# Performance work log

Hardware: AMD Instinct MI355X
Metric: run time of the kernel (lower is better)

Reference implementation:

```python
import jax, jax.numpy as jnp
import numpy as np

N_NODES = 100000
N_EDGES = 3200000
N_FEAT = 512
HIDDEN = 16
OUT_DIM = 1


def setup_inputs() -> dict:
    key = jax.random.key(0)
    ks = jax.random.split(key, 6)
    x = jax.random.normal(ks[0], (N_NODES, N_FEAT), dtype=jnp.float32)
    lap_vals = jax.random.uniform(ks[1], (N_EDGES,), dtype=jnp.float32)
    W1 = jax.random.normal(ks[2], (N_FEAT, HIDDEN), dtype=jnp.float32) * 0.05
    b1 = jnp.zeros((HIDDEN,), dtype=jnp.float32)
    W2 = jax.random.normal(ks[3], (HIDDEN, OUT_DIM), dtype=jnp.float32) * 0.05
    b2 = jnp.zeros((OUT_DIM,), dtype=jnp.float32)
    lap_rows = jax.random.randint(ks[4], (N_EDGES,), 0, N_NODES, dtype=jnp.int32)
    lap_cols = jax.random.randint(ks[5], (N_EDGES,), 0, N_NODES, dtype=jnp.int32)
    return {"x": x, "lap_vals": lap_vals, "W1": W1, "b1": b1,
            "W2": W2, "b2": b2, "lap_rows": lap_rows, "lap_cols": lap_cols}


def _spmm(vals, rows, cols, dense):
    # COO sparse [N,N] @ dense [N,D]: gather source rows, scale, scatter-add.
    return jax.ops.segment_sum(vals[:, None] * dense[cols], rows,
                               num_segments=N_NODES)


def reference(x, lap_vals, W1, b1, W2, b2, lap_rows, lap_cols):
    # Layer 1: dense GEMM -> sparse aggregation -> fused bias + relu
    h = jax.nn.relu(_spmm(lap_vals, lap_rows, lap_cols, x @ W1) + b1)
    # Layer 2: dense GEMM -> sparse aggregation -> fused bias + sigmoid
    out = jax.nn.sigmoid(_spmm(lap_vals, lap_rows, lap_cols, h @ W2) + b2)
    return out
```

## Files before the change

kernel.cpp:

```cpp
#include <hip/hip_runtime.h>
#include <cstdint>
#include <cstddef>

#define N_NODES 100000
#define N_EDGES 3200000
#define N_FEAT  512
#define HIDDEN  16
#define NBUCK   ((N_NODES + 127) / 128)
#define BCAP    5120
#define CHUNK   2048
#define NGB     ((N_NODES + 63) / 64)
#define NBS     ((N_EDGES + CHUNK - 1) / CHUNK)

static_assert(NGB == NBS, "parity interleave requires equal role counts");

__device__ __forceinline__ void gload_lds16(const float* g, void* lds) {
  __builtin_amdgcn_global_load_lds(
      (const __attribute__((address_space(1))) void*)g,
      (__attribute__((address_space(3))) void*)lds, 16, 0, 0);
}

__global__ __launch_bounds__(256)
void k_prep(int* __restrict__ cursor) {
  const int i = blockIdx.x * 256 + threadIdx.x;
  if (i < NBUCK) cursor[i] = 0;
}

__global__ __launch_bounds__(256)
void k_mega2(const float* __restrict__ x, const float* __restrict__ W1,
             float* __restrict__ xw, const int* __restrict__ rows,
             const int* __restrict__ cols, const float* __restrict__ vals,
             int* __restrict__ cursor, int2* __restrict__ binned) {
  __shared__ __align__(16) char smem[32768];
  const int t = threadIdx.x;

  if ((blockIdx.x & 1) == 0) {
    float4 (*xs)[2][256] = reinterpret_cast<float4 (*)[2][256]>(smem);
    const int l = t & 63;
    const int w = __builtin_amdgcn_readfirstlane(t >> 6);
    const int rbase = (blockIdx.x >> 1) * 64;
    const int kbase0 = w * 128;

    float acc[16];
#pragma unroll
    for (int c = 0; c < 16; ++c) acc[c] = 0.f;

    const int sq   = ((l & 3) ^ ((l >> 3) & 3)) * 4;
    const int srow = l >> 2;

    auto STAGE = [&](int b, int ck) {
      const int kb = kbase0 + ck * 16;
#pragma unroll
      for (int i = 0; i < 4; ++i) {
        int grow = rbase + i * 16 + srow;
        if (grow >= N_NODES) grow = N_NODES - 1;
        gload_lds16(x + (size_t)grow * N_FEAT + kb + sq, &xs[w][b][i * 64]);
      }
    };

    const int rsw = (l >> 1) & 3;
    auto COMPUTE = [&](int b, int ck) {
      const int kb = kbase0 + ck * 16;
#pragma unroll
      for (int q = 0; q < 4; ++q) {
        float4 xv = xs[w][b][l * 4 + (q ^ rsw)];
        float xe[4] = {xv.x, xv.y, xv.z, xv.w};
#pragma unroll
        for (int j = 0; j < 4; ++j) {
          const float* wrow = W1 + (size_t)(kb + q * 4 + j) * 16;
#pragma unroll
          for (int c = 0; c < 16; ++c)
            acc[c] = fmaf(xe[j], wrow[c], acc[c]);
        }
      }
    };

    STAGE(0, 0);
#pragma unroll 1
    for (int ck = 0; ck < 8; ++ck) {
      const int b = ck & 1;
      if (ck + 1 < 8) {
        STAGE(b ^ 1, ck + 1);
        asm volatile("s_waitcnt vmcnt(4)" ::: "memory");
      } else {
        asm volatile("s_waitcnt vmcnt(0)" ::: "memory");
      }
      COMPUTE(b, ck);
    }

    float4* red = &xs[w][0][0];
    red[l * 4 + 0] = make_float4(acc[0],  acc[1],  acc[2],  acc[3]);
    red[l * 4 + 1] = make_float4(acc[4],  acc[5],  acc[6],  acc[7]);
    red[l * 4 + 2] = make_float4(acc[8],  acc[9],  acc[10], acc[11]);
    red[l * 4 + 3] = make_float4(acc[12], acc[13], acc[14], acc[15]);
    __syncthreads();

    const int rr = t >> 2, qq = t & 3;
    const int grow = rbase + rr;
    if (grow < N_NODES) {
      const int s = rr * 4 + qq;
      float4 a = xs[0][0][s], b4 = xs[1][0][s], c4 = xs[2][0][s], d4 = xs[3][0][s];
      float4 o = make_float4(a.x + b4.x + c4.x + d4.x, a.y + b4.y + c4.y + d4.y,
                             a.z + b4.z + c4.z + d4.z, a.w + b4.w + c4.w + d4.w);
      ((float4*)xw)[(size_t)grow * 4 + qq] = o;
    }
  } else {
    int2*           stash = (int2*)smem;
    unsigned short* sbuck = (unsigned short*)(smem + 16384);
    int*            hist  = (int*)(smem + 16384 + 4096);
    int*            base  = (int*)(smem + 16384 + 4096 + 4 * NBUCK);
    const int e0 = (blockIdx.x >> 1) * CHUNK;
    const int nv = (N_EDGES - e0 < CHUNK) ? (N_EDGES - e0) : CHUNK;

    for (int b = t; b < NBUCK; b += 256) hist[b] = 0;
    __syncthreads();

#pragma unroll
    for (int i = 0; i < CHUNK / 256; ++i) {
      const int idx = i * 256 + t;
      if (idx < nv) {
        const int e = e0 + idx;
        const int r = rows[e], c = cols[e];
        const float v = vals[e];
        const int b = r >> 7;
        stash[idx] = make_int2(c | ((r & 127) << 20), __float_as_int(v));
        sbuck[idx] = (unsigned short)b;
        atomicAdd(&hist[b], 1);
      }
    }
    __syncthreads();

    for (int b = t; b < NBUCK; b += 256) {
      const int h = hist[b];
      base[b] = (h > 0) ? atomicAdd(&cursor[b], h) : 0;
      hist[b] = 0;
    }
    __syncthreads();

#pragma unroll
    for (int i = 0; i < CHUNK / 256; ++i) {
      const int idx = i * 256 + t;
      if (idx < nv) {
        const int b = sbuck[idx];
        const int off = base[b] + atomicAdd(&hist[b], 1);
        if (off < BCAP) binned[(size_t)b * BCAP + off] = stash[idx];
      }
    }
  }
}

__global__ __launch_bounds__(256)
void k_localcsr(const int2* __restrict__ binned, const int* __restrict__ cursor,
                int2* __restrict__ binned2, int* __restrict__ row_beg,
                int* __restrict__ row_end) {
  __shared__ unsigned short rk[BCAP];
  __shared__ int hist[128];
  __shared__ int pfx[128];
  const int t = threadIdx.x;
  const int b = blockIdx.x;
  const int raw = cursor[b];
  const int cnt = raw < BCAP ? raw : BCAP;
  const int2* ep = binned + (size_t)b * BCAP;
  int2* eq = binned2 + (size_t)b * BCAP;

  if (t < 128) hist[t] = 0;
  __syncthreads();

  for (int i = t; i < cnt; i += 256) {
    const int row = (ep[i].x >> 20) & 127;
    rk[i] = (unsigned short)atomicAdd(&hist[row], 1);
  }
  __syncthreads();

  if (t < 128) pfx[t] = hist[t];
  __syncthreads();
#pragma unroll
  for (int off = 1; off < 128; off <<= 1) {
    int add = (t >= off && t < 128) ? pfx[t - off] : 0;
    __syncthreads();
    if (t < 128) pfx[t] += add;
    __syncthreads();
  }

  if (t < 128) {
    const int r = b * 128 + t;
    if (r < N_NODES) {
      const int beg = b * BCAP + pfx[t] - hist[t];
      row_beg[r] = beg;
      row_end[r] = beg + hist[t];
    }
  }
  __syncthreads();

  for (int i = t; i < cnt; i += 256) {
    const int2 e = ep[i];
    const int row = (e.x >> 20) & 127;
    eq[pfx[row] - hist[row] + (int)rk[i]] = e;
  }
}

__global__ __launch_bounds__(256)
void k_fused1(const int2* __restrict__ binned2, const int* __restrict__ row_beg,
              const int* __restrict__ row_end, const float* __restrict__ xw,
              const float* __restrict__ b1, const float* __restrict__ W2,
              float* __restrict__ hw1) {
  const int t = threadIdx.x;
  const int lane16 = t & 15;
  const int r = blockIdx.x * 16 + (t >> 4);
  if (r >= N_NODES) return;
  const int s = row_beg[r], e = row_end[r];
  float a0 = 0.f, a1 = 0.f, a2 = 0.f, a3 = 0.f;
  int i = s;
  for (; i + 3 < e; i += 4) {
    int2 ea = binned2[i],     eb = binned2[i + 1];
    int2 ec = binned2[i + 2], ed = binned2[i + 3];
    a0 = fmaf(__int_as_float(ea.y), xw[(size_t)(ea.x & 0xFFFFF) * 16 + lane16], a0);
    a1 = fmaf(__int_as_float(eb.y), xw[(size_t)(eb.x & 0xFFFFF) * 16 + lane16], a1);
    a2 = fmaf(__int_as_float(ec.y), xw[(size_t)(ec.x & 0xFFFFF) * 16 + lane16], a2);
    a3 = fmaf(__int_as_float(ed.y), xw[(size_t)(ed.x & 0xFFFFF) * 16 + lane16], a3);
  }
  for (; i < e; ++i) {
    int2 ea = binned2[i];
    a0 = fmaf(__int_as_float(ea.y), xw[(size_t)(ea.x & 0xFFFFF) * 16 + lane16], a0);
  }
  float h = fmaxf((a0 + a1) + (a2 + a3) + b1[lane16], 0.f);
  float p = h * W2[lane16];
#pragma unroll
  for (int m = 8; m >= 1; m >>= 1) p += __shfl_xor(p, m, 16);
  if (lane16 == 0) hw1[r] = p;
}

__global__ __launch_bounds__(256)
void k_fused2(const int2* __restrict__ binned2, const int* __restrict__ row_beg,
              const int* __restrict__ row_end, const float* __restrict__ hw1,
              const float* __restrict__ b2, float* __restrict__ out) {
  const int t = threadIdx.x;
  const int lane16 = t & 15;
  const int r = blockIdx.x * 16 + (t >> 4);
  if (r >= N_NODES) return;
  const int s = row_beg[r], e = row_end[r];
  float acc = 0.f;
  for (int i = s + lane16; i < e; i += 16) {
    int2 ev = binned2[i];
    acc = fmaf(__int_as_float(ev.y), hw1[ev.x & 0xFFFFF], acc);
  }
#pragma unroll
  for (int m = 8; m >= 1; m >>= 1) acc += __shfl_xor(acc, m, 16);
  if (lane16 == 0) out[r] = 1.f / (1.f + expf(-(acc + b2[0])));
}

extern "C" void kernel_launch(void* const* d_in, const int* in_sizes, int n_in,
                              void* d_out, int out_size, void* d_ws, size_t ws_size,
                              hipStream_t stream) {
  const float* x    = (const float*)d_in[0];
  const float* vals = (const float*)d_in[1];
  const float* W1   = (const float*)d_in[2];
  const float* b1   = (const float*)d_in[3];
  const float* W2   = (const float*)d_in[4];
  const float* b2   = (const float*)d_in[5];
  const int*   rows = (const int*)d_in[6];
  const int*   cols = (const int*)d_in[7];
  float* out = (float*)d_out;

  char* w = (char*)d_ws;
  float* xw      = (float*)w;  w += (size_t)N_NODES * 16 * 4;
  int2*  binned  = (int2*)w;   w += (size_t)NBUCK * BCAP * 8;
  int2*  binned2 = (int2*)w;   w += (size_t)NBUCK * BCAP * 8;
  int*   cursor  = (int*)w;    w += (size_t)((NBUCK + 3) & ~3) * 4;
  int*   row_beg = (int*)w;    w += (size_t)N_NODES * 4;
  int*   row_end = (int*)w;    w += (size_t)N_NODES * 4;
  float* hw1     = (float*)w;

  k_prep    <<<(NBUCK + 255) / 256, 256, 0, stream>>>(cursor);
  k_mega2   <<<NGB + NBS,           256, 0, stream>>>(x, W1, xw, rows, cols, vals,
                                                      cursor, binned);
  k_localcsr<<<NBUCK,               256, 0, stream>>>(binned, cursor, binned2,
                                                      row_beg, row_end);
  k_fused1  <<<(N_NODES + 15) / 16, 256, 0, stream>>>(binned2, row_beg, row_end,
                                                      xw, b1, W2, hw1);
  k_fused2  <<<(N_NODES + 15) / 16, 256, 0, stream>>>(binned2, row_beg, row_end,
                                                      hw1, b2, out);
}
```

Measured before the change: 189.5 us.

## Fuse per-bucket CSR sort with layer-1 aggregation using LDS-staged edges

Merges the local CSR build and the first sparse aggregation into one kernel per 128-row bucket. Edges are sorted into an LDS stash and then aggregated straight from LDS, which removes one kernel launch and the global re-read of sorted edges. The sorted copy is still written to global memory for layer 2. It also shrinks the bucket capacity to 4608 so the int2 stash fits in LDS, which raises the risk of dropping edges in overfull buckets. The block grows to 512 threads, and only about 782 blocks now do the layer-1 gathers, so parallelism is lower.

```diff
diff --git a/kernel.cpp b/kernel.cpp
--- a/kernel.cpp
+++ b/kernel.cpp
@@ -7,10 +7,11 @@
 #define N_FEAT  512
 #define HIDDEN  16
 #define NBUCK   ((N_NODES + 127) / 128)
-#define BCAP    5120
+#define BCAP    4608
 #define CHUNK   2048
 #define NGB     ((N_NODES + 63) / 64)
 #define NBS     ((N_EDGES + CHUNK - 1) / CHUNK)
+#define AGG_T   512
 
 static_assert(NGB == NBS, "parity interleave requires equal role counts");
 
@@ -149,85 +150,87 @@
   }
 }
 
-__global__ __launch_bounds__(256)
-void k_localcsr(const int2* __restrict__ binned, const int* __restrict__ cursor,
-                int2* __restrict__ binned2, int* __restrict__ row_beg,
-                int* __restrict__ row_end) {
-  __shared__ unsigned short rk[BCAP];
+__global__ __launch_bounds__(AGG_T)
+void k_sortagg(const int2* __restrict__ binned, const int* __restrict__ cursor,
+               int2* __restrict__ binned2, int* __restrict__ row_beg,
+               int* __restrict__ row_end, const float* __restrict__ xw,
+               const float* __restrict__ b1, const float* __restrict__ W2,
+               float* __restrict__ hw1) {
+  __shared__ int2 stash[BCAP];
   __shared__ int hist[128];
-  __shared__ int pfx[128];
+  __shared__ int inc[128];
+  __shared__ int cnt2[128];
   const int t = threadIdx.x;
   const int b = blockIdx.x;
   const int raw = cursor[b];
   const int cnt = raw < BCAP ? raw : BCAP;
   const int2* ep = binned + (size_t)b * BCAP;
-  int2* eq = binned2 + (size_t)b * BCAP;
-
-  if (t < 128) hist[t] = 0;
-  __syncthreads();
-
-  for (int i = t; i < cnt; i += 256) {
-    const int row = (ep[i].x >> 20) & 127;
-    rk[i] = (unsigned short)atomicAdd(&hist[row], 1);
-  }
-  __syncthreads();
-
-  if (t < 128) pfx[t] = hist[t];
+
+  if (t < 128) { hist[t] = 0; cnt2[t] = 0; }
+  __syncthreads();
+
+  for (int i = t; i < cnt; i += AGG_T)
+    atomicAdd(&hist[(ep[i].x >> 20) & 127], 1);
+  __syncthreads();
+
+  if (t < 128) inc[t] = hist[t];
   __syncthreads();
 #pragma unroll
   for (int off = 1; off < 128; off <<= 1) {
-    int add = (t >= off && t < 128) ? pfx[t - off] : 0;
-    __syncthreads();
-    if (t < 128) pfx[t] += add;
+    int add = (t >= off && t < 128) ? inc[t - off] : 0;
+    __syncthreads();
+    if (t < 128) inc[t] += add;
     __syncthreads();
   }
 
   if (t < 128) {
     const int r = b * 128 + t;
     if (r < N_NODES) {
-      const int beg = b * BCAP + pfx[t] - hist[t];
-      row_beg[r] = beg;
-      row_end[r] = beg + hist[t];
-    }
-  }
-  __syncthreads();
-
-  for (int i = t; i < cnt; i += 256) {
+      row_beg[r] = b * BCAP + inc[t] - hist[t];
+      row_end[r] = b * BCAP + inc[t];
+    }
+  }
+
+  for (int i = t; i < cnt; i += AGG_T) {
     const int2 e = ep[i];
     const int row = (e.x >> 20) & 127;
-    eq[pfx[row] - hist[row] + (int)rk[i]] = e;
-  }
-}
-
-__global__ __launch_bounds__(256)
-void k_fused1(const int2* __restrict__ binned2, const int* __restrict__ row_beg,
-              const int* __restrict__ row_end, const float* __restrict__ xw,
-              const float* __restrict__ b1, const float* __restrict__ W2,
-              float* __restrict__ hw1) {
-  const int t = threadIdx.x;
+    const int off = inc[row] - hist[row] + atomicAdd(&cnt2[row], 1);
+    stash[off] = e;
+  }
+  __syncthreads();
+
+  int2* eq = binned2 + (size_t)b * BCAP;
+  for (int i = t; i < cnt; i += AGG_T) eq[i] = stash[i];
+
   const int lane16 = t & 15;
-  const int r = blockIdx.x * 16 + (t >> 4);
-  if (r >= N_NODES) return;
-  const int s = row_beg[r], e = row_end[r];
-  float a0 = 0.f, a1 = 0.f, a2 = 0.f, a3 = 0.f;
-  int i = s;
-  for (; i + 3 < e; i += 4) {
-    int2 ea = binned2[i],     eb = binned2[i + 1];
-    int2 ec = binned2[i + 2], ed = binned2[i + 3];
-    a0 = fmaf(__int_as_float(ea.y), xw[(size_t)(ea.x & 0xFFFFF) * 16 + lane16], a0);
-    a1 = fmaf(__int_as_float(eb.y), xw[(size_t)(eb.x & 0xFFFFF) * 16 + lane16], a1);
-    a2 = fmaf(__int_as_float(ec.y), xw[(size_t)(ec.x & 0xFFFFF) * 16 + lane16], a2);
-    a3 = fmaf(__int_as_float(ed.y), xw[(size_t)(ed.x & 0xFFFFF) * 16 + lane16], a3);
-  }
-  for (; i < e; ++i) {
-    int2 ea = binned2[i];
-    a0 = fmaf(__int_as_float(ea.y), xw[(size_t)(ea.x & 0xFFFFF) * 16 + lane16], a0);
-  }
-  float h = fmaxf((a0 + a1) + (a2 + a3) + b1[lane16], 0.f);
-  float p = h * W2[lane16];
-#pragma unroll
-  for (int m = 8; m >= 1; m >>= 1) p += __shfl_xor(p, m, 16);
-  if (lane16 == 0) hw1[r] = p;
+  const int g = t >> 4;
+  const float bb = b1[lane16];
+  const float ww = W2[lane16];
+#pragma unroll 1
+  for (int rr = g; rr < 128; rr += 32) {
+    const int r = b * 128 + rr;
+    if (r >= N_NODES) continue;
+    const int s = inc[rr] - hist[rr], e2 = inc[rr];
+    float a0 = 0.f, a1 = 0.f, a2 = 0.f, a3 = 0.f;
+    int i = s;
+    for (; i + 3 < e2; i += 4) {
+      int2 ea = stash[i],     eb = stash[i + 1];
+      int2 ec = stash[i + 2], ed = stash[i + 3];
+      a0 = fmaf(__int_as_float(ea.y), xw[(size_t)(ea.x & 0xFFFFF) * 16 + lane16], a0);
+      a1 = fmaf(__int_as_float(eb.y), xw[(size_t)(eb.x & 0xFFFFF) * 16 + lane16], a1);
+      a2 = fmaf(__int_as_float(ec.y), xw[(size_t)(ec.x & 0xFFFFF) * 16 + lane16], a2);
+      a3 = fmaf(__int_as_float(ed.y), xw[(size_t)(ed.x & 0xFFFFF) * 16 + lane16], a3);
+    }
+    for (; i < e2; ++i) {
+      int2 ea = stash[i];
+      a0 = fmaf(__int_as_float(ea.y), xw[(size_t)(ea.x & 0xFFFFF) * 16 + lane16], a0);
+    }
+    float h = fmaxf((a0 + a1) + (a2 + a3) + bb, 0.f);
+    float p = h * ww;
+#pragma unroll
+    for (int m = 8; m >= 1; m >>= 1) p += __shfl_xor(p, m, 16);
+    if (lane16 == 0) hw1[r] = p;
+  }
 }
 
 __global__ __launch_bounds__(256)
@@ -271,13 +274,12 @@
   int*   row_end = (int*)w;    w += (size_t)N_NODES * 4;
   float* hw1     = (float*)w;
 
-  k_prep    <<<(NBUCK + 255) / 256, 256, 0, stream>>>(cursor);
-  k_mega2   <<<NGB + NBS,           256, 0, stream>>>(x, W1, xw, rows, cols, vals,
-                                                      cursor, binned);
-  k_localcsr<<<NBUCK,               256, 0, stream>>>(binned, cursor, binned2,
-                                                      row_beg, row_end);
-  k_fused1  <<<(N_NODES + 15) / 16, 256, 0, stream>>>(binned2, row_beg, row_end,
-                                                      xw, b1, W2, hw1);
-  k_fused2  <<<(N_NODES + 15) / 16, 256, 0, stream>>>(binned2, row_beg, row_end,
-                                                      hw1, b2, out);
-}
+  k_prep    <<<(NBUCK + 255) / 256, 256,   0, stream>>>(cursor);
+  k_mega2   <<<NGB + NBS,           256,   0, stream>>>(x, W1, xw, rows, cols,
+                                                        vals, cursor, binned);
+  k_sortagg <<<NBUCK,               AGG_T, 0, stream>>>(binned, cursor, binned2,
+                                                        row_beg, row_end, xw,
+                                                        b1, W2, hw1);
+  k_fused2  <<<(N_NODES + 15) / 16, 256,   0, stream>>>(binned2, row_beg, row_end,
+                                                        hw1, b2, out);
+}
```

Measured after the change: 155.5 us. 1.22x faster.
